# Kernel optimization log

Measured on AMD Instinct MI355X. Metric: run time of the kernel, lower is better.

Reference implementation:

```python
import jax, jax.numpy as jnp
import numpy as np

B, S, D = 4, 4096, 1024
H, F = 16, 256
HD = D // H  # 64


def setup_inputs() -> dict:
    key = jax.random.key(0)
    ks = jax.random.split(key, 10)
    scale = 1.0 / np.sqrt(D)
    x = jax.random.normal(ks[0], (B, S, D), dtype=jnp.float32)
    Wq = jax.random.normal(ks[1], (D, D), dtype=jnp.float32) * scale
    bq = jnp.zeros((D,), dtype=jnp.float32)
    Wk = jax.random.normal(ks[2], (D, D), dtype=jnp.float32) * scale
    bk = jnp.zeros((D,), dtype=jnp.float32)
    Wv = jax.random.normal(ks[3], (D, D), dtype=jnp.float32) * scale
    bv = jnp.zeros((D,), dtype=jnp.float32)
    Wo = jax.random.normal(ks[4], (D, D), dtype=jnp.float32) * scale
    bo = jnp.zeros((D,), dtype=jnp.float32)
    rf = jax.random.normal(ks[5], (H, HD, F), dtype=jnp.float32) / np.sqrt(F)
    return {"x": x, "Wq": Wq, "bq": bq, "Wk": Wk, "bk": bk,
            "Wv": Wv, "bv": bv, "Wo": Wo, "bo": bo, "rf": rf}


def _heads(y):
    # [B,S,D] -> [B,H,S,HD]
    return y.reshape(B, S, H, HD).transpose(0, 2, 1, 3)


def reference(x, Wq, bq, Wk, bk, Wv, bv, Wo, bo, rf):
    q = _heads(x @ Wq.T + bq)
    k = _heads(x @ Wk.T + bk)
    v = _heads(x @ Wv.T + bv)
    # positive feature maps: softplus(random projection)
    q_prime = jax.nn.softplus(jnp.einsum('bhsd,hdf->bhsf', q, rf))
    k_prime = jax.nn.softplus(jnp.einsum('bhsd,hdf->bhsf', k, rf))
    kv = jnp.einsum('bhsf,bhsd->bhfd', k_prime, v)          # [B,H,F,HD]
    k_sum = k_prime.sum(axis=2)                              # [B,H,F]
    qkv = jnp.einsum('bhsf,bhfd->bhsd', q_prime, kv)        # [B,H,S,HD]
    denom = jnp.einsum('bhsf,bhf->bhs', q_prime, k_sum) + 1e-8
    out = qkv / denom[..., None]
    out = out.transpose(0, 2, 1, 3).reshape(B, S, D)
    return out @ Wo.T + bo
```

## Files before the change

kernel.cpp:

```cpp
#include <hip/hip_runtime.h>
#include <hip/hip_bf16.h>
#include <math.h>

#define Bb 4
#define Ss 4096
#define Dd 1024
#define Hh 16
#define Ff 256
#define HDd 64
#define Mm (Bb*Ss)

typedef unsigned int u32;
typedef unsigned short u16;

typedef __attribute__((ext_vector_type(8))) short bf16x8;
typedef __attribute__((ext_vector_type(4))) float f32x4;

__device__ __forceinline__ float bflo(u32 u){ union{u32 i; float f;} c; c.i = u << 16; return c.f; }
__device__ __forceinline__ float bfhi(u32 u){ union{u32 i; float f;} c; c.i = u & 0xffff0000u; return c.f; }
__device__ __forceinline__ u16 f2b(float f){
  union{float f; u32 i;} c; c.f = f;
  u32 x = c.i;
  return (u16)((x + 0x7fffu + ((x >> 16) & 1u)) >> 16);
}
__device__ __forceinline__ u32 pk2(float lo, float hi){
  union { __hip_bfloat162 h; u32 u; } c;
  c.h = __float22bfloat162_rn(make_float2(lo, hi));
  return c.u;
}
__device__ __forceinline__ float sfast(float x){
  return fmaxf(x, 0.f) + __logf(1.f + __expf(-fabsf(x)));
}
__device__ __forceinline__ void gload_lds16(const u16* g, u16* l){
  __builtin_amdgcn_global_load_lds(
      (const __attribute__((address_space(1))) void*)g,
      (__attribute__((address_space(3))) void*)l, 16, 0, 0);
}

__global__ void cvt_bf16(const float* __restrict__ in, u16* __restrict__ out, int n)
{
  int i = (blockIdx.x * 256 + threadIdx.x) * 8;
  if (i >= n) return;
  float4 a = *reinterpret_cast<const float4*>(in + i);
  float4 b = *reinterpret_cast<const float4*>(in + i + 4);
  *reinterpret_cast<uint4*>(out + i) =
      make_uint4(pk2(a.x, a.y), pk2(a.z, a.w), pk2(b.x, b.y), pk2(b.z, b.w));
}

__global__ void zero_f32(float* __restrict__ p, int n)
{
  int i = blockIdx.x * 256 + threadIdx.x;
  if (i < n) p[i] = 0.f;
}

template<typename OT, bool BROW>
__global__ __launch_bounds__(256, 2) void mfma_gemm_bt(
    const u16* __restrict__ A, const u16* __restrict__ W,
    const float* __restrict__ bias, OT* __restrict__ C,
    int M, int N, int K)
{
  __shared__ __align__(16) u16 As[128 * 32];
  __shared__ __align__(16) u16 Bs[128 * 32];

  const int tid = threadIdx.x;
  const int wave = tid >> 6, lane = tid & 63;
  const int quad = lane >> 4, lm = lane & 15;
  const int wm = (wave >> 1) * 64, wn = (wave & 1) * 64;
  const int m0 = blockIdx.x * 128, n0 = blockIdx.y * 128;

  f32x4 acc[4][4] = {};

  for (int k0 = 0; k0 < K; k0 += 32) {
#pragma unroll
    for (int j = 0; j < 2; j++) {
      const int c = wave * 128 + j * 64 + lane;
      const int r = c >> 2, cg = c & 3;
      u16* ldsA = &As[(wave * 128 + j * 64) * 8];
      u16* ldsB = &Bs[(wave * 128 + j * 64) * 8];
      gload_lds16(A + (size_t)(m0 + r) * K + k0 + cg * 8, ldsA);
      gload_lds16(W + (size_t)(n0 + r) * K + k0 + cg * 8, ldsB);
    }
    __syncthreads();

    bf16x8 af[4], bf[4];
#pragma unroll
    for (int mi = 0; mi < 4; mi++)
      af[mi] = *reinterpret_cast<const bf16x8*>(&As[(wm + mi * 16 + lm) * 32 + quad * 8]);
#pragma unroll
    for (int ni = 0; ni < 4; ni++)
      bf[ni] = *reinterpret_cast<const bf16x8*>(&Bs[(wn + ni * 16 + lm) * 32 + quad * 8]);
#pragma unroll
    for (int mi = 0; mi < 4; mi++)
#pragma unroll
      for (int ni = 0; ni < 4; ni++)
        acc[mi][ni] = __builtin_amdgcn_mfma_f32_16x16x32_bf16(af[mi], bf[ni], acc[mi][ni], 0, 0, 0);
    __syncthreads();
  }

#pragma unroll
  for (int mi = 0; mi < 4; mi++)
#pragma unroll
    for (int ni = 0; ni < 4; ni++) {
      const int n = n0 + wn + ni * 16 + lm;
      const float bvn = BROW ? 0.f : bias[n];
#pragma unroll
      for (int r = 0; r < 4; r++) {
        const int m = m0 + wm + mi * 16 + quad * 4 + r;
        const float val = acc[mi][ni][r] + (BROW ? bias[m] : bvn);
        if constexpr (sizeof(OT) == 2) ((u16*)C)[(size_t)m * N + n] = f2b(val);
        else                           ((float*)C)[(size_t)m * N + n] = val;
      }
    }
}

__global__ void rf_transpose(const float* __restrict__ rf, float* __restrict__ rft)
{
  const int h = blockIdx.x, d = blockIdx.y, f = threadIdx.x;
  rft[((size_t)h * Ff + f) * HDd + d] = rf[((size_t)(h * HDd + d)) * Ff + f];
}

#define NSPLIT 8
#define SCHUNKS (Ss / NSPLIT / 64)

__global__ __launch_bounds__(256, 2) void kv_fused(
    const u16* __restrict__ Km, const u16* __restrict__ Vt,
    const float* __restrict__ rft, float* __restrict__ kv, float* __restrict__ ksum)
{
  __shared__ __align__(16) u16 KSd[2][64 * 64];
  __shared__ __align__(16) u16 VSd[2][64 * 64];
  __shared__ __align__(16) u16 PT[4][64 * 64];

  const int bh = blockIdx.x;
  const int b = bh >> 4, h = bh & 15;
  const int s0 = blockIdx.y * (Ss / NSPLIT);
  const int tid = threadIdx.x;
  const int wave = tid >> 6, lane = tid & 63;
  const int quad = lane >> 4, lm = lane & 15;
  const int F0 = wave * 64;

  bf16x8 bfr[4][2];
  {
    const float* rh = rft + (size_t)h * Ff * HDd;
#pragma unroll
    for (int ni = 0; ni < 4; ni++) {
      const float* rrow = rh + (size_t)(F0 + ni * 16 + lm) * HDd;
#pragma unroll
      for (int ks = 0; ks < 2; ks++) {
        float4 a = *reinterpret_cast<const float4*>(rrow + ks * 32 + quad * 8);
        float4 e = *reinterpret_cast<const float4*>(rrow + ks * 32 + quad * 8 + 4);
        union { u32 w[4]; bf16x8 v; } u;
        u.w[0] = pk2(a.x, a.y); u.w[1] = pk2(a.z, a.w);
        u.w[2] = pk2(e.x, e.y); u.w[3] = pk2(e.z, e.w);
        bfr[ni][ks] = u.v;
      }
    }
  }

  const int j0 = wave * 64 + lane, j1 = j0 + 256;
  const int r0 = j0 >> 3, c0 = (j0 & 7) ^ (r0 & 7);
  const int r1 = j1 >> 3, c1 = (j1 & 7) ^ (r1 & 7);

  auto KV_STAGE = [&](int buf, int ch) {
    const int sc = s0 + ch * 64;
    gload_lds16(Km + (size_t)(b * Ss + sc + r0) * Dd + h * 64 + c0 * 8, &KSd[buf][(wave * 64) * 8]);
    gload_lds16(Km + (size_t)(b * Ss + sc + r1) * Dd + h * 64 + c1 * 8, &KSd[buf][(wave * 64 + 256) * 8]);
    gload_lds16(Vt + (size_t)(h * 64 + r0) * Mm + b * Ss + sc + c0 * 8, &VSd[buf][(wave * 64) * 8]);
    gload_lds16(Vt + (size_t)(h * 64 + r1) * Mm + b * Ss + sc + c1 * 8, &VSd[buf][(wave * 64 + 256) * 8]);
  };

  f32x4 kvacc[4][4] = {};
  float kss[4] = {0.f, 0.f, 0.f, 0.f};

  KV_STAGE(0, 0);

#pragma unroll
  for (int ch = 0; ch < SCHUNKS; ch++) {
    const int cur = ch & 1;
    if (ch + 1 < SCHUNKS) {
      KV_STAGE(cur ^ 1, ch + 1);
      asm volatile("s_waitcnt vmcnt(4)" ::: "memory");
    } else {
      asm volatile("s_waitcnt vmcnt(0)" ::: "memory");
    }
    __builtin_amdgcn_s_barrier();
    __builtin_amdgcn_sched_barrier(0);

    const u16* KSc = &KSd[cur][0];
    const u16* VSc = &VSd[cur][0];

    f32x4 p[4][4] = {};
#pragma unroll
    for (int ks2 = 0; ks2 < 2; ks2++) {
      bf16x8 af[4];
#pragma unroll
      for (int mi = 0; mi < 4; mi++) {
        int row = mi * 16 + lm;
        af[mi] = *reinterpret_cast<const bf16x8*>(
            (const char*)KSc + row * 128 + (((ks2 * 4 + quad) ^ (row & 7)) * 16));
      }
#pragma unroll
      for (int mi = 0; mi < 4; mi++)
#pragma unroll
        for (int ni = 0; ni < 4; ni++)
          p[mi][ni] = __builtin_amdgcn_mfma_f32_16x16x32_bf16(af[mi], bfr[ni][ks2], p[mi][ni], 0, 0, 0);
    }

#pragma unroll
    for (int mi = 0; mi < 4; mi++)
#pragma unroll
      for (int ni = 0; ni < 4; ni++) {
        float v0 = sfast(p[mi][ni][0]);
        float v1 = sfast(p[mi][ni][1]);
        float v2 = sfast(p[mi][ni][2]);
        float v3 = sfast(p[mi][ni][3]);
        kss[ni] += (v0 + v1) + (v2 + v3);
        int row = ni * 16 + lm;
        int off = (row * 128 + mi * 32 + quad * 8) ^ ((row & 7) << 4);
        *reinterpret_cast<uint2*>((char*)&PT[wave][0] + off) =
            make_uint2(pk2(v0, v1), pk2(v2, v3));
      }

#pragma unroll
    for (int ks2 = 0; ks2 < 2; ks2++) {
      bf16x8 a2[4], b2[4];
#pragma unroll
      for (int mi = 0; mi < 4; mi++) {
        int row = mi * 16 + lm;
        a2[mi] = *reinterpret_cast<const bf16x8*>(
            (char*)&PT[wave][0] + row * 128 + (((ks2 * 4 + quad) ^ (row & 7)) * 16));
      }
#pragma unroll
      for (int ni = 0; ni < 4; ni++) {
        int row = ni * 16 + lm;
        b2[ni] = *reinterpret_cast<const bf16x8*>(
            (const char*)VSc + row * 128 + (((ks2 * 4 + quad) ^ (row & 7)) * 16));
      }
#pragma unroll
      for (int mi = 0; mi < 4; mi++)
#pragma unroll
        for (int ni = 0; ni < 4; ni++)
          kvacc[mi][ni] = __builtin_amdgcn_mfma_f32_16x16x32_bf16(a2[mi], b2[ni], kvacc[mi][ni], 0, 0, 0);
    }

    __builtin_amdgcn_sched_barrier(0);
    __builtin_amdgcn_s_barrier();
  }

  float* kvp = kv + (size_t)bh * Ff * HDd;
#pragma unroll
  for (int mi = 0; mi < 4; mi++)
#pragma unroll
    for (int ni = 0; ni < 4; ni++)
#pragma unroll
      for (int rr = 0; rr < 4; rr++) {
        int f = F0 + mi * 16 + quad * 4 + rr;
        int d = ni * 16 + lm;
        atomicAdd(kvp + (size_t)f * HDd + d, kvacc[mi][ni][rr]);
      }
#pragma unroll
  for (int ni = 0; ni < 4; ni++) {
    float v = kss[ni];
    v += __shfl_xor(v, 16, 64);
    v += __shfl_xor(v, 32, 64);
    if (quad == 0) atomicAdd(ksum + (size_t)bh * Ff + F0 + ni * 16 + lm, v);
  }
}

__global__ void kvt_cvt(const float* __restrict__ kv, u16* __restrict__ kvtb)
{
  const int bh = blockIdx.x;
  const int d = threadIdx.x & 63, fg = threadIdx.x >> 6;
  const float* src = kv + (size_t)bh * Ff * HDd + d;
  u32* dst = reinterpret_cast<u32*>(kvtb + (size_t)bh * HDd * Ff + (size_t)d * Ff + fg * 64);
#pragma unroll
  for (int j = 0; j < 32; j++) {
    float v0 = src[(size_t)(fg * 64 + 2 * j) * HDd];
    float v1 = src[(size_t)(fg * 64 + 2 * j + 1) * HDd];
    dst[j] = pk2(v0, v1);
  }
}

#define ASPLIT 16
#define ACHUNKS (Ss / ASPLIT / 64)

__global__ __launch_bounds__(256, 2) void attn_fused(
    const u16* __restrict__ Qm, const float* __restrict__ rft,
    const u16* __restrict__ kvtb, const float* __restrict__ ksum,
    u16* __restrict__ attnb)
{
  __shared__ __align__(16) u16 P4[4][64 * 64];
  __shared__ __align__(16) float den4[64][4];

  const int bh = blockIdx.x;
  const int b = bh >> 4, h = bh & 15;
  const int s0 = blockIdx.y * (Ss / ASPLIT);
  const int tid = threadIdx.x;
  const int wave = tid >> 6, lane = tid & 63;
  const int quad = lane >> 4, lm = lane & 15;
  const int F0 = wave * 64;

  bf16x8 bfr[4][2];
  {
    const float* rh = rft + (size_t)h * Ff * HDd;
#pragma unroll
    for (int ni = 0; ni < 4; ni++) {
      const float* rrow = rh + (size_t)(F0 + ni * 16 + lm) * HDd;
#pragma unroll
      for (int ks = 0; ks < 2; ks++) {
        float4 a = *reinterpret_cast<const float4*>(rrow + ks * 32 + quad * 8);
        float4 e = *reinterpret_cast<const float4*>(rrow + ks * 32 + quad * 8 + 4);
        union { u32 w[4]; bf16x8 v; } u;
        u.w[0] = pk2(a.x, a.y); u.w[1] = pk2(a.z, a.w);
        u.w[2] = pk2(e.x, e.y); u.w[3] = pk2(e.z, e.w);
        bfr[ni][ks] = u.v;
      }
    }
  }
  bf16x8 b2r[4][2];
  {
    const u16* kb = kvtb + (size_t)bh * HDd * Ff + (size_t)(wave * 16 + lm) * Ff;
#pragma unroll
    for (int fb = 0; fb < 4; fb++)
#pragma unroll
      for (int k2 = 0; k2 < 2; k2++)
        b2r[fb][k2] = *reinterpret_cast<const bf16x8*>(kb + fb * 64 + k2 * 32 + quad * 8);
  }
  float ksv[4];
#pragma unroll
  for (int ni = 0; ni < 4; ni++)
    ksv[ni] = ksum[(size_t)bh * Ff + F0 + ni * 16 + lm];

  for (int ch = 0; ch < ACHUNKS; ch++) {
    const int sc0 = s0 + ch * 64;

    bf16x8 af[4][2];
#pragma unroll
    for (int mi = 0; mi < 4; mi++) {
      const u16* qrow = Qm + (size_t)(b * Ss + sc0 + mi * 16 + lm) * Dd + h * 64;
#pragma unroll
      for (int ks = 0; ks < 2; ks++)
        af[mi][ks] = *reinterpret_cast<const bf16x8*>(qrow + ks * 32 + quad * 8);
    }
    f32x4 p[4][4] = {};
#pragma unroll
    for (int ks = 0; ks < 2; ks++)
#pragma unroll
      for (int mi = 0; mi < 4; mi++)
#pragma unroll
        for (int ni = 0; ni < 4; ni++)
          p[mi][ni] = __builtin_amdgcn_mfma_f32_16x16x32_bf16(af[mi][ks], bfr[ni][ks], p[mi][ni], 0, 0, 0);

#pragma unroll
    for (int mi = 0; mi < 4; mi++) {
      const int sbase = mi * 16 + quad * 4;
      float dd[4] = {0.f, 0.f, 0.f, 0.f};
#pragma unroll
      for (int ni = 0; ni < 4; ni++) {
        u32 pk01 = pk2(sfast(p[mi][ni][0]), sfast(p[mi][ni][1]));
        u32 pk23 = pk2(sfast(p[mi][ni][2]), sfast(p[mi][ni][3]));
        dd[0] += bflo(pk01) * ksv[ni];
        dd[1] += bfhi(pk01) * ksv[ni];
        dd[2] += bflo(pk23) * ksv[ni];
        dd[3] += bfhi(pk23) * ksv[ni];
        u32 ob01 = (u32)__shfl_xor((int)pk01, 1, 64);
        u32 ob23 = (u32)__shfl_xor((int)pk23, 1, 64);
        const int odd = lm & 1;
        u32 w_a = odd ? ((ob23 & 0xffffu) | (pk23 << 16))
                      : ((pk01 & 0xffffu) | (ob01 << 16));
        u32 w_b = odd ? ((ob23 >> 16)     | (pk23 & 0xffff0000u))
                      : ((pk01 >> 16)     | (ob01 & 0xffff0000u));
        const int row_a = sbase + (odd ? 2 : 0);
        const int row_b = sbase + (odd ? 3 : 1);
        const int fpb = ni * 16 + (lm & ~1);
        const int cc = fpb >> 3;
        const int bib = (fpb & 7) * 2;
        *reinterpret_cast<u32*>((char*)&P4[wave][0] + row_a * 128 + ((cc ^ (row_a & 7)) << 4) + bib) = w_a;
        *reinterpret_cast<u32*>((char*)&P4[wave][0] + row_b * 128 + ((cc ^ (row_b & 7)) << 4) + bib) = w_b;
      }
#pragma unroll
      for (int r = 0; r < 4; r++) {
        float v = dd[r];
        v += __shfl_xor(v, 1, 64);
        v += __shfl_xor(v, 2, 64);
        v += __shfl_xor(v, 4, 64);
        v += __shfl_xor(v, 8, 64);
        if (lm == 0) den4[sbase + r][wave] = v;
      }
    }
    __syncthreads();

    f32x4 acc2[4] = {};
#pragma unroll
    for (int fb = 0; fb < 4; fb++)
#pragma unroll
      for (int k2 = 0; k2 < 2; k2++) {
        bf16x8 af2[4];
#pragma unroll
        for (int mi = 0; mi < 4; mi++) {
          int row = mi * 16 + lm;
          af2[mi] = *reinterpret_cast<const bf16x8*>(
              (char*)&P4[fb][0] + row * 128 + (((k2 * 4 + quad) ^ (row & 7)) << 4));
        }
#pragma unroll
        for (int mi = 0; mi < 4; mi++)
          acc2[mi] = __builtin_amdgcn_mfma_f32_16x16x32_bf16(af2[mi], b2r[fb][k2], acc2[mi], 0, 0, 0);
      }

#pragma unroll
    for (int mi = 0; mi < 4; mi++) {
#pragma unroll
      for (int r = 0; r < 4; r++) {
        const int s = mi * 16 + quad * 4 + r;
        float4 dv = *reinterpret_cast<const float4*>(&den4[s][0]);
        const float inv = 1.f / ((dv.x + dv.y) + (dv.z + dv.w) + 1e-8f);
        attnb[(size_t)(b * Ss + sc0 + s) * Dd + h * 64 + wave * 16 + lm] =
            f2b(acc2[mi][r] * inv);
      }
    }
    __syncthreads();
  }
}

extern "C" void kernel_launch(void* const* d_in, const int* in_sizes, int n_in,
                              void* d_out, int out_size, void* d_ws, size_t ws_size,
                              hipStream_t stream)
{
  const float* x  = (const float*)d_in[0];
  const float* Wq = (const float*)d_in[1];
  const float* bq = (const float*)d_in[2];
  const float* Wk = (const float*)d_in[3];
  const float* bk = (const float*)d_in[4];
  const float* Wv = (const float*)d_in[5];
  const float* bv = (const float*)d_in[6];
  const float* Wo = (const float*)d_in[7];
  const float* bo = (const float*)d_in[8];
  const float* rf = (const float*)d_in[9];

  char* w = (char*)d_ws;
  u16* xb = (u16*)w;        w += (size_t)Mm * Dd * 2;
  u16* q  = (u16*)w;        w += (size_t)Mm * Dd * 2;
  u16* k  = (u16*)w;        w += (size_t)Mm * Dd * 2;
  u16* vt = (u16*)w;        w += (size_t)Mm * Dd * 2;
  u16* wqb = (u16*)w;       w += (size_t)Dd * Dd * 2;
  u16* wkb = (u16*)w;       w += (size_t)Dd * Dd * 2;
  u16* wvb = (u16*)w;       w += (size_t)Dd * Dd * 2;
  u16* wob = (u16*)w;       w += (size_t)Dd * Dd * 2;
  float* kv = (float*)w;    w += (size_t)(Bb * Hh) * Ff * HDd * 4;
  float* ks = (float*)w;    w += (size_t)(Bb * Hh) * Ff * 4;
  float* rft = (float*)w;   w += (size_t)Hh * Ff * HDd * 4;
  u16* kvtb = wqb;

  cvt_bf16<<<(Mm * Dd / 8 + 255) / 256, 256, 0, stream>>>(x, xb, Mm * Dd);
  cvt_bf16<<<(Dd * Dd / 8 + 255) / 256, 256, 0, stream>>>(Wq, wqb, Dd * Dd);
  cvt_bf16<<<(Dd * Dd / 8 + 255) / 256, 256, 0, stream>>>(Wk, wkb, Dd * Dd);
  cvt_bf16<<<(Dd * Dd / 8 + 255) / 256, 256, 0, stream>>>(Wv, wvb, Dd * Dd);
  cvt_bf16<<<(Dd * Dd / 8 + 255) / 256, 256, 0, stream>>>(Wo, wob, Dd * Dd);

  const int nz = (Bb * Hh) * Ff * HDd + (Bb * Hh) * Ff;
  zero_f32<<<(nz + 255) / 256, 256, 0, stream>>>(kv, nz);
  rf_transpose<<<dim3(Hh, HDd), 256, 0, stream>>>(rf, rft);

  const dim3 gg(Mm / 128, Dd / 128);
  mfma_gemm_bt<u16, false><<<gg, 256, 0, stream>>>(xb, wqb, bq, q, Mm, Dd, Dd);
  mfma_gemm_bt<u16, false><<<gg, 256, 0, stream>>>(xb, wkb, bk, k, Mm, Dd, Dd);
  const dim3 gv(Dd / 128, Mm / 128);
  mfma_gemm_bt<u16, true><<<gv, 256, 0, stream>>>(wvb, xb, bv, vt, Dd, Mm, Dd);

  kv_fused<<<dim3(Bb * Hh, NSPLIT), 256, 0, stream>>>(k, vt, rft, kv, ks);

  kvt_cvt<<<Bb * Hh, 256, 0, stream>>>(kv, kvtb);

  attn_fused<<<dim3(Bb * Hh, ASPLIT), 256, 0, stream>>>(q, rft, kvtb, ks, xb);

  mfma_gemm_bt<float, false><<<gg, 256, 0, stream>>>(xb, wob, bo, (float*)d_out, Mm, Dd, Dd);
}
```

Measured before the change: 568.7 us.

## Drop double buffering in kv_fused, doubling sequence split and shrinking register use

The kv_fused kernel now uses single K/V LDS buffers with plain __syncthreads instead of a double-buffered async prefetch pipeline. NSPLIT goes from 8 to 16, and the projection/softplus loop is restructured per mi row so only four accumulators stay live, lowering register pressure. It also adds #pragma unroll 1. The aim is to raise occupancy and parallelism, giving up load/compute overlap and doubling the number of atomic adds for the kv reduction.

```diff
diff --git a/kernel.cpp b/kernel.cpp
--- a/kernel.cpp
+++ b/kernel.cpp
@@ -119,15 +119,15 @@
   rft[((size_t)h * Ff + f) * HDd + d] = rf[((size_t)(h * HDd + d)) * Ff + f];
 }
 
-#define NSPLIT 8
+#define NSPLIT 16
 #define SCHUNKS (Ss / NSPLIT / 64)
 
 __global__ __launch_bounds__(256, 2) void kv_fused(
     const u16* __restrict__ Km, const u16* __restrict__ Vt,
     const float* __restrict__ rft, float* __restrict__ kv, float* __restrict__ ksum)
 {
-  __shared__ __align__(16) u16 KSd[2][64 * 64];
-  __shared__ __align__(16) u16 VSd[2][64 * 64];
+  __shared__ __align__(16) u16 KS[64 * 64];
+  __shared__ __align__(16) u16 VS[64 * 64];
   __shared__ __align__(16) u16 PT[4][64 * 64];
 
   const int bh = blockIdx.x;
@@ -160,65 +160,43 @@
   const int r0 = j0 >> 3, c0 = (j0 & 7) ^ (r0 & 7);
   const int r1 = j1 >> 3, c1 = (j1 & 7) ^ (r1 & 7);
 
-  auto KV_STAGE = [&](int buf, int ch) {
-    const int sc = s0 + ch * 64;
-    gload_lds16(Km + (size_t)(b * Ss + sc + r0) * Dd + h * 64 + c0 * 8, &KSd[buf][(wave * 64) * 8]);
-    gload_lds16(Km + (size_t)(b * Ss + sc + r1) * Dd + h * 64 + c1 * 8, &KSd[buf][(wave * 64 + 256) * 8]);
-    gload_lds16(Vt + (size_t)(h * 64 + r0) * Mm + b * Ss + sc + c0 * 8, &VSd[buf][(wave * 64) * 8]);
-    gload_lds16(Vt + (size_t)(h * 64 + r1) * Mm + b * Ss + sc + c1 * 8, &VSd[buf][(wave * 64 + 256) * 8]);
-  };
-
   f32x4 kvacc[4][4] = {};
   float kss[4] = {0.f, 0.f, 0.f, 0.f};
 
-  KV_STAGE(0, 0);
-
-#pragma unroll
+#pragma unroll 1
   for (int ch = 0; ch < SCHUNKS; ch++) {
-    const int cur = ch & 1;
-    if (ch + 1 < SCHUNKS) {
-      KV_STAGE(cur ^ 1, ch + 1);
-      asm volatile("s_waitcnt vmcnt(4)" ::: "memory");
-    } else {
-      asm volatile("s_waitcnt vmcnt(0)" ::: "memory");
-    }
-    __builtin_amdgcn_s_barrier();
-    __builtin_amdgcn_sched_barrier(0);
-
-    const u16* KSc = &KSd[cur][0];
-    const u16* VSc = &VSd[cur][0];
-
-    f32x4 p[4][4] = {};
-#pragma unroll
-    for (int ks2 = 0; ks2 < 2; ks2++) {
-      bf16x8 af[4];
-#pragma unroll
-      for (int mi = 0; mi < 4; mi++) {
-        int row = mi * 16 + lm;
-        af[mi] = *reinterpret_cast<const bf16x8*>(
-            (const char*)KSc + row * 128 + (((ks2 * 4 + quad) ^ (row & 7)) * 16));
-      }
-#pragma unroll
-      for (int mi = 0; mi < 4; mi++)
+    const int sc = s0 + ch * 64;
+    gload_lds16(Km + (size_t)(b * Ss + sc + r0) * Dd + h * 64 + c0 * 8, &KS[(wave * 64) * 8]);
+    gload_lds16(Km + (size_t)(b * Ss + sc + r1) * Dd + h * 64 + c1 * 8, &KS[(wave * 64 + 256) * 8]);
+    gload_lds16(Vt + (size_t)(h * 64 + r0) * Mm + b * Ss + sc + c0 * 8, &VS[(wave * 64) * 8]);
+    gload_lds16(Vt + (size_t)(h * 64 + r1) * Mm + b * Ss + sc + c1 * 8, &VS[(wave * 64 + 256) * 8]);
+    __syncthreads();
+
+#pragma unroll
+    for (int mi = 0; mi < 4; mi++) {
+      const int row = mi * 16 + lm;
+      f32x4 pmi[4] = {};
+#pragma unroll
+      for (int ks2 = 0; ks2 < 2; ks2++) {
+        bf16x8 af = *reinterpret_cast<const bf16x8*>(
+            (const char*)KS + row * 128 + (((ks2 * 4 + quad) ^ (row & 7)) * 16));
 #pragma unroll
         for (int ni = 0; ni < 4; ni++)
-          p[mi][ni] = __builtin_amdgcn_mfma_f32_16x16x32_bf16(af[mi], bfr[ni][ks2], p[mi][ni], 0, 0, 0);
-    }
-
-#pragma unroll
-    for (int mi = 0; mi < 4; mi++)
+          pmi[ni] = __builtin_amdgcn_mfma_f32_16x16x32_bf16(af, bfr[ni][ks2], pmi[ni], 0, 0, 0);
+      }
 #pragma unroll
       for (int ni = 0; ni < 4; ni++) {
-        float v0 = sfast(p[mi][ni][0]);
-        float v1 = sfast(p[mi][ni][1]);
-        float v2 = sfast(p[mi][ni][2]);
-        float v3 = sfast(p[mi][ni][3]);
+        float v0 = sfast(pmi[ni][0]);
+        float v1 = sfast(pmi[ni][1]);
+        float v2 = sfast(pmi[ni][2]);
+        float v3 = sfast(pmi[ni][3]);
         kss[ni] += (v0 + v1) + (v2 + v3);
-        int row = ni * 16 + lm;
-        int off = (row * 128 + mi * 32 + quad * 8) ^ ((row & 7) << 4);
+        int frow = ni * 16 + lm;
+        int off = (frow * 128 + mi * 32 + quad * 8) ^ ((frow & 7) << 4);
         *reinterpret_cast<uint2*>((char*)&PT[wave][0] + off) =
             make_uint2(pk2(v0, v1), pk2(v2, v3));
       }
+    }
 
 #pragma unroll
     for (int ks2 = 0; ks2 < 2; ks2++) {
@@ -233,7 +211,7 @@
       for (int ni = 0; ni < 4; ni++) {
         int row = ni * 16 + lm;
         b2[ni] = *reinterpret_cast<const bf16x8*>(
-            (const char*)VSc + row * 128 + (((ks2 * 4 + quad) ^ (row & 7)) * 16));
+            (const char*)VS + row * 128 + (((ks2 * 4 + quad) ^ (row & 7)) * 16));
       }
 #pragma unroll
       for (int mi = 0; mi < 4; mi++)
@@ -241,9 +219,7 @@
         for (int ni = 0; ni < 4; ni++)
           kvacc[mi][ni] = __builtin_amdgcn_mfma_f32_16x16x32_bf16(a2[mi], b2[ni], kvacc[mi][ni], 0, 0, 0);
     }
-
-    __builtin_amdgcn_sched_barrier(0);
-    __builtin_amdgcn_s_barrier();
+    __syncthreads();
   }
 
   float* kvp = kv + (size_t)bh * Ff * HDd;
```

Result: faster. 505.8 us (-11.1%).
